# Performance work log

Hardware: AMD Instinct MI355X
Metric: run time of the kernel (lower is better)

## Reference

```python
import jax, jax.numpy as jnp
import numpy as np
from jax import lax

B, N, S, H = 8, 32, 512, 768   # batch, max spans, seq len, bert hidden
K, C, L = 3, 128, 64           # conv kernel height, cnn_hidden_size, num labels


def setup_inputs() -> dict:
    key = jax.random.key(0)
    ks = jax.random.split(key, 9)
    rng = np.random.default_rng(0)
    W = 16  # max span width
    starts = rng.integers(0, S - W, size=(B, N))
    widths = rng.integers(1, W + 1, size=(B, N))
    starts[0, 0], widths[0, 0] = 100, W        # force max span width = 16
    starts[0, 1], widths[0, 1] = S - W, 1      # force max prefix width = 496
    starts[0, 2], widths[0, 2] = 0, 1          # force min end = 1 -> max suffix = 511
    ends = starts + widths
    spans_dranges = jnp.asarray(np.stack([starts, ends], axis=-1), dtype=jnp.int32)
    sc = 0.02
    return {
        "tokens_emb": jax.random.normal(ks[0], (B, S, H), jnp.float32),
        "span_w": jax.random.normal(ks[1], (C, H, K), jnp.float32) * sc,
        "span_b": jax.random.normal(ks[2], (C,), jnp.float32) * sc,
        "prefix_w": jax.random.normal(ks[3], (C, H, K), jnp.float32) * sc,
        "prefix_b": jax.random.normal(ks[4], (C,), jnp.float32) * sc,
        "suffix_w": jax.random.normal(ks[5], (C, H, K), jnp.float32) * sc,
        "suffix_b": jax.random.normal(ks[6], (C,), jnp.float32) * sc,
        "fc_w": jax.random.normal(ks[7], (L, 3 * C), jnp.float32) * sc,
        "fc_b": jax.random.normal(ks[8], (L,), jnp.float32) * sc,
        "spans_dranges": spans_dranges,
        "word_seq_lengths": jnp.full((B,), S, dtype=jnp.int32),
        "max_span_width": W,
        "max_prefix_width": S - W,
        "max_suffix_width": S - 1,
    }


def _conv_pool(x, w, b):
    # x: [BN, T, H]; Conv2d(H->C, kernel (K,1)) over time + max_pool over all valid positions
    T = x.shape[1]
    if T < K:  # original pads with zeros up to kernel size
        x = jnp.pad(x, ((0, 0), (0, K - T), (0, 0)))
    y = lax.conv_general_dilated(x.transpose(0, 2, 1), w, (1,), 'VALID',
                                 dimension_numbers=('NCH', 'OIH', 'NCH'))  # [BN, C, T-K+1]
    return (y + b[None, :, None]).max(axis=2)  # pool_filter_size == full output length


def reference(tokens_emb, span_w, span_b, prefix_w, prefix_b, suffix_w, suffix_b,
              fc_w, fc_b, spans_dranges, word_seq_lengths,
              max_span_width, max_prefix_width, max_suffix_width):
    starts = spans_dranges[..., 0]  # [B,N]
    ends = spans_dranges[..., 1]

    def gather(idx, mask):
        # idx, mask: [B,N,W] -> zero-padded per-span token embeddings [B*N, W, H]
        g = jnp.take_along_axis(tokens_emb[:, None], jnp.clip(idx, 0, S - 1)[..., None], axis=2)
        return (g * mask[..., None]).reshape(B * N, -1, H)

    ar = jnp.arange(max_span_width)
    span_x = gather(starts[..., None] + ar, ar < (ends - starts)[..., None])
    arp = jnp.arange(max_prefix_width)
    prefix_x = gather(jnp.broadcast_to(arp, (B, N, max_prefix_width)), arp < starts[..., None])
    ars = jnp.arange(max_suffix_width)
    suffix_x = gather(ends[..., None] + ars,
                      ars < (word_seq_lengths[:, None, None] - ends[..., None]))

    feats = jnp.concatenate([
        _conv_pool(prefix_x, prefix_w, prefix_b),
        _conv_pool(span_x, span_w, span_b),
        _conv_pool(suffix_x, suffix_w, suffix_b),
    ], axis=-1)  # [B*N, 3C]
    probs = jax.nn.sigmoid(feats @ fc_w.T + fc_b)  # [B*N, L]
    pred_ids = (probs > 0.5).astype(jnp.int32).reshape(B, N, L)
    return probs, pred_ids
```

## Files before the change

### kernel.cpp

```cpp
#include <hip/hip_runtime.h>
#include <hip/hip_bf16.h>
#include <math.h>

#define NEG_INF (-1e30f)

typedef _Float16 half8 __attribute__((ext_vector_type(8)));
typedef _Float16 half4 __attribute__((ext_vector_type(4)));
typedef float f32x4 __attribute__((ext_vector_type(4)));
typedef float f32x16 __attribute__((ext_vector_type(16)));

__device__ __forceinline__ void load_lds16(const void* g, void* l) {
  __builtin_amdgcn_global_load_lds((const __attribute__((address_space(1))) void*)g,
                                   (__attribute__((address_space(3))) void*)l, 16, 0, 0);
}

__global__ __launch_bounds__(256) void prep(
    const float* __restrict__ tokens, const float* __restrict__ span_w,
    const float* __restrict__ prefix_w, const float* __restrict__ suffix_w,
    const float* __restrict__ fc_w, _Float16* __restrict__ A2,
    _Float16* __restrict__ Bt, float* __restrict__ fcT) {
  int bid = blockIdx.x;
  int t = threadIdx.x;
  if (bid < 3072) {
    int g4 = (bid * 256 + t) * 4;
    int m = g4 / 768, h = g4 % 768;
    float4 x = *(const float4*)(tokens + g4);
    float xs[4] = {x.x, x.y, x.z, x.w};
    half4 hi, lo;
#pragma unroll
    for (int i = 0; i < 4; ++i) {
      _Float16 h_ = (_Float16)xs[i];
      hi[i] = h_;
      lo[i] = (_Float16)((xs[i] - (float)h_) * 64.0f);
    }
    size_t base = (size_t)m * 1536 + h;
    *(half4*)(A2 + base) = hi;
    *(half4*)(A2 + base + 768) = lo;
  } else if (bid < 3216) {
    int g = (bid - 3072) * 256 + t;
    int ws = g / 12288;
    int r = g % 12288;
    int c = r / 96, h = (r % 96) * 8;
    const float* wsrc = (ws == 0) ? prefix_w : (ws == 1) ? span_w : suffix_w;
    const float* src = wsrc + (size_t)(c * 768 + h) * 3;
    float wv[24];
#pragma unroll
    for (int i = 0; i < 6; ++i) *(float4*)&wv[i * 4] = *(const float4*)(src + i * 4);
#pragma unroll
    for (int tap = 0; tap < 3; ++tap) {
      half8 hi, lo;
#pragma unroll
      for (int i = 0; i < 8; ++i) {
        float x = wv[i * 3 + tap];
        _Float16 h_ = (_Float16)x;
        hi[i] = h_;
        lo[i] = (_Float16)((x - (float)h_) * 64.0f);
      }
      size_t jb = (size_t)(ws * 384 + tap * 128 + c) * 1536 + h;
      *(half8*)(Bt + jb) = hi;
      *(half8*)(Bt + jb + 768) = lo;
    }
  } else {
    int g = (bid - 3216) * 256 + t;
    int i = g >> 6, c = g & 63;
    fcT[g] = fc_w[c * 384 + i];
  }
}

__global__ __launch_bounds__(512) void gemm_f16(const _Float16* __restrict__ A2,
                                                const _Float16* __restrict__ Bt,
                                                float* __restrict__ Ct) {
  __shared__ _Float16 As[3][128 * 64];
  __shared__ _Float16 Bs[3][64 * 64];
  const int bm = blockIdx.x * 128;
  const int bj = blockIdx.y * 64;
  const int tid = threadIdx.x;
  const int w = tid >> 6;
  const int lane = tid & 63;
  const int lrow = lane >> 3;
  const int cphys = lane & 7;
  const int clog = cphys ^ (lrow & 7);
  const int srcoff = (clog >> 2) * 768 + (clog & 3) * 8;
  const _Float16* gA0 = A2 + (size_t)(bm + w * 16 + lrow) * 1536 + srcoff;
  const _Float16* gA1 = A2 + (size_t)(bm + w * 16 + 8 + lrow) * 1536 + srcoff;
  const _Float16* gB0 = Bt + (size_t)(bj + w * 8 + lrow) * 1536 + srcoff;
  const int m0w = (w & 3) * 32;
  const int n0w = (w >> 2) * 32;
  const int arow = m0w + (lane & 31);
  const int brow = n0w + (lane & 31);
  const int hi32 = lane >> 5;
  const int sw = lane & 7;
#define CO(p, ks) (((((p) * 4 + (ks) * 2 + hi32)) ^ sw) * 8)
#define STAGE(sb, t)                             \
  do {                                           \
    const int kp_ = (t) * 32;                    \
    load_lds16(gA0 + kp_, &As[(sb)][w * 1024]);  \
    load_lds16(gA1 + kp_, &As[(sb)][w * 1024 + 512]); \
    load_lds16(gB0 + kp_, &Bs[(sb)][w * 512]);   \
  } while (0)
  f32x16 aa, ab;
#pragma unroll
  for (int q = 0; q < 16; ++q) {
    aa[q] = 0.f;
    ab[q] = 0.f;
  }
  STAGE(0, 0);
  STAGE(1, 1);
  asm volatile("s_waitcnt vmcnt(3)" ::: "memory");
  __builtin_amdgcn_s_barrier();

  int cur = 0, sbuf = 2;
  for (int t = 0; t < 24; ++t) {
    if (t + 2 < 24) STAGE(sbuf, t + 2);
#pragma unroll
    for (int ks = 0; ks < 2; ++ks) {
      half8 a0 = *(const half8*)&As[cur][arow * 64 + CO(0, ks)];
      half8 a1 = *(const half8*)&As[cur][arow * 64 + CO(1, ks)];
      half8 b0 = *(const half8*)&Bs[cur][brow * 64 + CO(0, ks)];
      half8 b1 = *(const half8*)&Bs[cur][brow * 64 + CO(1, ks)];
      aa = __builtin_amdgcn_mfma_f32_32x32x16_f16(a0, b0, aa, 0, 0, 0);
      ab = __builtin_amdgcn_mfma_f32_32x32x16_f16(a1, b0, ab, 0, 0, 0);
      ab = __builtin_amdgcn_mfma_f32_32x32x16_f16(a0, b1, ab, 0, 0, 0);
    }
    if (t < 23) {
      asm volatile("s_waitcnt lgkmcnt(0)" ::: "memory");
      if (t < 22) {
        asm volatile("s_waitcnt vmcnt(3)" ::: "memory");
      } else {
        asm volatile("s_waitcnt vmcnt(0)" ::: "memory");
      }
      __builtin_amdgcn_s_barrier();
    }
    cur = (cur == 2) ? 0 : cur + 1;
    sbuf = (sbuf == 2) ? 0 : sbuf + 1;
  }
#undef STAGE
#undef CO
  const int n_out = bj + n0w + (lane & 31);
  float* cp = Ct + (size_t)n_out * 4096 + bm + m0w + 4 * hi32;
#pragma unroll
  for (int r = 0; r < 4; ++r) {
    f32x4 v;
#pragma unroll
    for (int q = 0; q < 4; ++q) v[q] = aa[4 * r + q] + 0.015625f * ab[4 * r + q];
    *(f32x4*)(cp + 8 * r) = v;
  }
}

__global__ __launch_bounds__(256) void scan_kernel(const float* __restrict__ Ct,
                                                   const int* __restrict__ wsl,
                                                   float* __restrict__ PM2,
                                                   float* __restrict__ SM2) {
  int pair = blockIdx.x * 4 + (threadIdx.x >> 6);
  int b = pair >> 7;
  int c = pair & 127;
  int lane = threadIdx.x & 63;
  int mb = b * 512;
  int t0 = lane * 8;
  const float* p0 = Ct + (size_t)(0 + c) * 4096 + mb;
  const float* p1 = Ct + (size_t)(128 + c) * 4096 + mb;
  const float* p2 = Ct + (size_t)(256 + c) * 4096 + mb;
  float v[8];
#pragma unroll
  for (int i = 0; i < 8; i++) {
    int t = t0 + i;
    v[i] = (t < 494) ? (p0[t] + p1[t + 1] + p2[t + 2]) : NEG_INF;
  }
#pragma unroll
  for (int i = 1; i < 8; i++) v[i] = fmaxf(v[i], v[i - 1]);
  float x = v[7];
#pragma unroll
  for (int d = 1; d < 64; d <<= 1) {
    float y = __shfl_up(x, d);
    if (lane >= d) x = fmaxf(x, y);
  }
  float excl = __shfl_up(x, 1);
  if (lane == 0) excl = NEG_INF;
  float* pm = PM2 + (size_t)pair * 512;
#pragma unroll
  for (int i = 0; i < 8; i++) {
    int t = t0 + i;
    if (t < 494) pm[t] = fmaxf(v[i], excl);
  }
  const float* s0 = Ct + (size_t)(768 + c) * 4096 + mb;
  const float* s1 = Ct + (size_t)(896 + c) * 4096 + mb;
  const float* s2 = Ct + (size_t)(1024 + c) * 4096 + mb;
  int qmax = wsl[b] - 3;
  if (qmax > 509) qmax = 509;
  float u[8];
#pragma unroll
  for (int i = 0; i < 8; i++) {
    int q = t0 + i;
    u[i] = (q <= qmax) ? (s0[q] + s1[q + 1] + s2[q + 2]) : NEG_INF;
  }
#pragma unroll
  for (int i = 6; i >= 0; i--) u[i] = fmaxf(u[i], u[i + 1]);
  float xr = u[0];
#pragma unroll
  for (int d = 1; d < 64; d <<= 1) {
    float y = __shfl_down(xr, d);
    if (lane < 64 - d) xr = fmaxf(xr, y);
  }
  float exclr = __shfl_down(xr, 1);
  if (lane == 63) exclr = NEG_INF;
  float* sm = SM2 + (size_t)pair * 512;
#pragma unroll
  for (int i = 0; i < 8; i++) sm[t0 + i] = fmaxf(u[i], exclr);
}

__global__ __launch_bounds__(128) void span_kernel(
    const float* __restrict__ Ct, const float* __restrict__ PM2,
    const float* __restrict__ SM2, const float* __restrict__ prefix_b,
    const float* __restrict__ span_b, const float* __restrict__ suffix_b,
    const float* __restrict__ fcT, const float* __restrict__ fc_b,
    const int* __restrict__ spans, const int* __restrict__ wsl,
    float* __restrict__ out) {
  __shared__ float sfeat[384];
  __shared__ float part[64];
  int sp = blockIdx.x;
  int b = sp >> 5;
  int c = threadIdx.x;
  int s = spans[sp * 2], e = spans[sp * 2 + 1];
  int Lb = wsl[b];
  int mb = b * 512;
  {
    const float* t0p = Ct + (size_t)c * 4096 + mb;
    const float* t1p = Ct + (size_t)(128 + c) * 4096 + mb;
    float m = NEG_INF;
    if (s >= 3) m = fmaxf(m, PM2[(size_t)(b * 128 + c) * 512 + s - 3]);
    if (s >= 2 && s <= 495) m = fmaxf(m, t0p[s - 2] + t1p[s - 1]);
    if (s >= 1 && s <= 494) m = fmaxf(m, t0p[s - 1]);
    if (s <= 493) m = fmaxf(m, 0.0f);
    sfeat[c] = m + prefix_b[c];
  }
  {
    const float* u0 = Ct + (size_t)(384 + c) * 4096 + mb;
    const float* u1 = Ct + (size_t)(512 + c) * 4096 + mb;
    const float* u2 = Ct + (size_t)(640 + c) * 4096 + mb;
    int w = e - s;
    float m = NEG_INF;
    for (int p = 0; p + 2 < w; ++p)
      m = fmaxf(m, u0[s + p] + u1[s + p + 1] + u2[s + p + 2]);
    if (w >= 2 && w <= 15) m = fmaxf(m, u0[s + w - 2] + u1[s + w - 1]);
    if (w <= 14) m = fmaxf(m, u0[s + w - 1]);
    if (w <= 13) m = fmaxf(m, 0.0f);
    sfeat[128 + c] = m + span_b[c];
  }
  {
    const float* x0 = Ct + (size_t)(768 + c) * 4096 + mb;
    const float* x1 = Ct + (size_t)(896 + c) * 4096 + mb;
    float m = NEG_INF;
    if (e <= Lb - 3) m = fmaxf(m, SM2[(size_t)(b * 128 + c) * 512 + e]);
    if (Lb - 2 - e >= 0 && Lb - 2 - e <= 508)
      m = fmaxf(m, x0[Lb - 2] + x1[Lb - 1]);
    if (Lb - 1 - e >= 0 && Lb - 1 - e <= 508) m = fmaxf(m, x0[Lb - 1]);
    if (Lb - e <= 508) m = fmaxf(m, 0.0f);
    sfeat[256 + c] = m + suffix_b[c];
  }
  __syncthreads();
  {
    int cc = threadIdx.x & 63;
    int half = threadIdx.x >> 6;
    float acc2 = 0.0f;
    const float* fp = fcT + (size_t)(half * 192) * 64 + cc;
    const float* sf = sfeat + half * 192;
#pragma unroll 8
    for (int i = 0; i < 192; ++i) acc2 = fmaf(sf[i], fp[(size_t)i * 64], acc2);
    if (half) part[cc] = acc2;
    __syncthreads();
    if (!half) {
      float a = acc2 + part[cc] + fc_b[cc];
      float pr = 1.0f / (1.0f + expf(-a));
      out[sp * 64 + cc] = pr;
      out[16384 + sp * 64 + cc] = (pr > 0.5f) ? 1.0f : 0.0f;
    }
  }
}

extern "C" void kernel_launch(void* const* d_in, const int* in_sizes, int n_in,
                              void* d_out, int out_size, void* d_ws,
                              size_t ws_size, hipStream_t stream) {
  const float* tokens = (const float*)d_in[0];
  const float* span_w = (const float*)d_in[1];
  const float* span_b = (const float*)d_in[2];
  const float* prefix_w = (const float*)d_in[3];
  const float* prefix_b = (const float*)d_in[4];
  const float* suffix_w = (const float*)d_in[5];
  const float* suffix_b = (const float*)d_in[6];
  const float* fc_w = (const float*)d_in[7];
  const float* fc_b = (const float*)d_in[8];
  const int* spans = (const int*)d_in[9];
  const int* wsl = (const int*)d_in[10];
  float* out = (float*)d_out;

  char* ws = (char*)d_ws;
  float* Ct = (float*)ws;
  _Float16* A2 = (_Float16*)(ws + 18874368);
  _Float16* Bt = (_Float16*)(ws + 31457280);
  float* PM2 = (float*)(ws + 34996224);
  float* SM2 = (float*)(ws + 37093376);
  float* fcT = (float*)(ws + 39190528);

  hipLaunchKernelGGL(prep, dim3(3312), dim3(256), 0, stream, tokens, span_w,
                     prefix_w, suffix_w, fc_w, A2, Bt, fcT);
  hipLaunchKernelGGL(gemm_f16, dim3(32, 18), dim3(512), 0, stream, A2, Bt, Ct);
  hipLaunchKernelGGL(scan_kernel, dim3(256), dim3(256), 0, stream, Ct, wsl,
                     PM2, SM2);
  hipLaunchKernelGGL(span_kernel, dim3(256), dim3(128), 0, stream, Ct, PM2,
                     SM2, prefix_b, span_b, suffix_b, fcT, fc_b, spans, wsl,
                     out);
}
```

Before: 155.5 us.

## Pre-tile GEMM operands in prep and switch GEMM to double-buffered LDS

The prep kernel now writes the fp16 hi/lo split of the tokens and conv weights in a tiled layout (k-group major, 8-element rows per M/N index), staging the token tile through LDS. This lets the GEMM load contiguous 512-element chunks per wave without an XOR swizzle. The GEMM drops from triple to double buffering, reads all fragments before a barrier, then issues the next stage's loads and runs the MFMAs at raised priority. The intent is to cut LDS bank conflicts and address arithmetic and to overlap loads with compute, at the cost of an extra barrier per iteration and a heavier prep kernel.

```diff
diff --git a/kernel.cpp b/kernel.cpp
--- a/kernel.cpp
+++ b/kernel.cpp
@@ -14,38 +14,56 @@
                                    (__attribute__((address_space(3))) void*)l, 16, 0, 0);
 }
 
+
 __global__ __launch_bounds__(256) void prep(
     const float* __restrict__ tokens, const float* __restrict__ span_w,
     const float* __restrict__ prefix_w, const float* __restrict__ suffix_w,
-    const float* __restrict__ fc_w, _Float16* __restrict__ A2,
-    _Float16* __restrict__ Bt, float* __restrict__ fcT) {
+    const float* __restrict__ fc_w, _Float16* __restrict__ A2t,
+    _Float16* __restrict__ Btt, float* __restrict__ fcT) {
+  __shared__ _Float16 lds[16 * 1544];
   int bid = blockIdx.x;
   int t = threadIdx.x;
-  if (bid < 3072) {
-    int g4 = (bid * 256 + t) * 4;
-    int m = g4 / 768, h = g4 % 768;
-    float4 x = *(const float4*)(tokens + g4);
-    float xs[4] = {x.x, x.y, x.z, x.w};
-    half4 hi, lo;
-#pragma unroll
-    for (int i = 0; i < 4; ++i) {
-      _Float16 h_ = (_Float16)xs[i];
-      hi[i] = h_;
-      lo[i] = (_Float16)((xs[i] - (float)h_) * 64.0f);
-    }
-    size_t base = (size_t)m * 1536 + h;
-    *(half4*)(A2 + base) = hi;
-    *(half4*)(A2 + base + 768) = lo;
-  } else if (bid < 3216) {
-    int g = (bid - 3072) * 256 + t;
+  if (bid < 256) {
+    int m0 = bid * 16;
+#pragma unroll
+    for (int r = 0; r < 12; ++r) {
+      int idx4 = r * 256 + t;
+      int ml = idx4 / 192;
+      int hh = (idx4 % 192) * 4;
+      float4 x = *(const float4*)(tokens + (size_t)m0 * 768 + (size_t)idx4 * 4);
+      float xs[4] = {x.x, x.y, x.z, x.w};
+#pragma unroll
+      for (int i = 0; i < 4; ++i) {
+        _Float16 h_ = (_Float16)xs[i];
+        lds[ml * 1544 + hh + i] = h_;
+        lds[ml * 1544 + 768 + hh + i] = (_Float16)((xs[i] - (float)h_) * 64.0f);
+      }
+    }
+    __syncthreads();
+#pragma unroll
+    for (int rep = 0; rep < 12; ++rep) {
+      int tg = rep * 16 + (t >> 4);
+      int ml = t & 15;
+      int g = tg & 7;
+      int tt = tg >> 3;
+      int p = g >> 2, ks = (g >> 1) & 1, h2 = g & 1;
+      int ksrc = tt * 32 + ks * 16 + h2 * 8;
+      half8 v = *(const half8*)&lds[ml * 1544 + p * 768 + ksrc];
+      *(half8*)(A2t + ((size_t)tg * 4096 + m0 + ml) * 8) = v;
+    }
+  } else if (bid < 400) {
+    int g = (bid - 256) * 256 + t;
     int ws = g / 12288;
     int r = g % 12288;
-    int c = r / 96, h = (r % 96) * 8;
+    int h8 = r >> 7, c = r & 127;
+    int h0 = h8 * 8;
     const float* wsrc = (ws == 0) ? prefix_w : (ws == 1) ? span_w : suffix_w;
-    const float* src = wsrc + (size_t)(c * 768 + h) * 3;
+    const float* src = wsrc + ((size_t)c * 768 + h0) * 3;
     float wv[24];
 #pragma unroll
     for (int i = 0; i < 6; ++i) *(float4*)&wv[i * 4] = *(const float4*)(src + i * 4);
+    int tt = h0 >> 5, ks = (h0 >> 4) & 1, h2 = (h0 >> 3) & 1;
+    int g_hi = ks * 2 + h2;
 #pragma unroll
     for (int tap = 0; tap < 3; ++tap) {
       half8 hi, lo;
@@ -56,48 +74,59 @@
         hi[i] = h_;
         lo[i] = (_Float16)((x - (float)h_) * 64.0f);
       }
-      size_t jb = (size_t)(ws * 384 + tap * 128 + c) * 1536 + h;
-      *(half8*)(Bt + jb) = hi;
-      *(half8*)(Bt + jb + 768) = lo;
+      int j = ws * 384 + tap * 128 + c;
+      *(half8*)(Btt + ((size_t)(tt * 8 + g_hi) * 1152 + j) * 8) = hi;
+      *(half8*)(Btt + ((size_t)(tt * 8 + g_hi + 4) * 1152 + j) * 8) = lo;
     }
   } else {
-    int g = (bid - 3216) * 256 + t;
+    int g = (bid - 400) * 256 + t;
     int i = g >> 6, c = g & 63;
     fcT[g] = fc_w[c * 384 + i];
   }
 }
 
-__global__ __launch_bounds__(512) void gemm_f16(const _Float16* __restrict__ A2,
-                                                const _Float16* __restrict__ Bt,
+__global__ __launch_bounds__(512) void gemm_f16(const _Float16* __restrict__ A2t,
+                                                const _Float16* __restrict__ Btt,
                                                 float* __restrict__ Ct) {
-  __shared__ _Float16 As[3][128 * 64];
-  __shared__ _Float16 Bs[3][64 * 64];
+  __shared__ _Float16 S[2][12288];
   const int bm = blockIdx.x * 128;
   const int bj = blockIdx.y * 64;
   const int tid = threadIdx.x;
   const int w = tid >> 6;
   const int lane = tid & 63;
-  const int lrow = lane >> 3;
-  const int cphys = lane & 7;
-  const int clog = cphys ^ (lrow & 7);
-  const int srcoff = (clog >> 2) * 768 + (clog & 3) * 8;
-  const _Float16* gA0 = A2 + (size_t)(bm + w * 16 + lrow) * 1536 + srcoff;
-  const _Float16* gA1 = A2 + (size_t)(bm + w * 16 + 8 + lrow) * 1536 + srcoff;
-  const _Float16* gB0 = Bt + (size_t)(bj + w * 8 + lrow) * 1536 + srcoff;
+  const int u0 = w * 3;
+  const _Float16* su[3];
+  size_t ts[3];
+  int du[3];
+#pragma unroll
+  for (int i = 0; i < 3; ++i) {
+    int u = u0 + i;
+    du[i] = u * 512;
+    if (u < 16) {
+      su[i] = A2t + (size_t)(u >> 1) * 32768 + ((size_t)bm + (u & 1) * 64 + lane) * 8;
+      ts[i] = 262144;
+    } else {
+      su[i] = Btt + (size_t)(u - 16) * 9216 + ((size_t)bj + lane) * 8;
+      ts[i] = 73728;
+    }
+  }
+  const _Float16* su0 = su[0];
+  const _Float16* su1 = su[1];
+  const _Float16* su2 = su[2];
+  const size_t ts0 = ts[0], ts1 = ts[1], ts2 = ts[2];
+  const int du0 = du[0], du1 = du[1], du2 = du[2];
+#define STAGE(buf, t)                                      \
+  do {                                                     \
+    load_lds16(su0 + (size_t)(t) * ts0, &S[(buf)][du0]);   \
+    load_lds16(su1 + (size_t)(t) * ts1, &S[(buf)][du1]);   \
+    load_lds16(su2 + (size_t)(t) * ts2, &S[(buf)][du2]);   \
+  } while (0)
+  const int ln31 = lane & 31;
+  const int hi32 = lane >> 5;
   const int m0w = (w & 3) * 32;
   const int n0w = (w >> 2) * 32;
-  const int arow = m0w + (lane & 31);
-  const int brow = n0w + (lane & 31);
-  const int hi32 = lane >> 5;
-  const int sw = lane & 7;
-#define CO(p, ks) (((((p) * 4 + (ks) * 2 + hi32)) ^ sw) * 8)
-#define STAGE(sb, t)                             \
-  do {                                           \
-    const int kp_ = (t) * 32;                    \
-    load_lds16(gA0 + kp_, &As[(sb)][w * 1024]);  \
-    load_lds16(gA1 + kp_, &As[(sb)][w * 1024 + 512]); \
-    load_lds16(gB0 + kp_, &Bs[(sb)][w * 512]);   \
-  } while (0)
+  const int aoff = (m0w + ln31) * 8;
+  const int boff = 8192 + (n0w + ln31) * 8;
   f32x16 aa, ab;
 #pragma unroll
   for (int q = 0; q < 16; ++q) {
@@ -107,36 +136,42 @@
   STAGE(0, 0);
   STAGE(1, 1);
   asm volatile("s_waitcnt vmcnt(3)" ::: "memory");
-  __builtin_amdgcn_s_barrier();
-
-  int cur = 0, sbuf = 2;
+  asm volatile("s_barrier" ::: "memory");
+
   for (int t = 0; t < 24; ++t) {
-    if (t + 2 < 24) STAGE(sbuf, t + 2);
+    const int cur = t & 1;
+    half8 a0[2], a1[2], b0[2], b1[2];
 #pragma unroll
     for (int ks = 0; ks < 2; ++ks) {
-      half8 a0 = *(const half8*)&As[cur][arow * 64 + CO(0, ks)];
-      half8 a1 = *(const half8*)&As[cur][arow * 64 + CO(1, ks)];
-      half8 b0 = *(const half8*)&Bs[cur][brow * 64 + CO(0, ks)];
-      half8 b1 = *(const half8*)&Bs[cur][brow * 64 + CO(1, ks)];
-      aa = __builtin_amdgcn_mfma_f32_32x32x16_f16(a0, b0, aa, 0, 0, 0);
-      ab = __builtin_amdgcn_mfma_f32_32x32x16_f16(a1, b0, ab, 0, 0, 0);
-      ab = __builtin_amdgcn_mfma_f32_32x32x16_f16(a0, b1, ab, 0, 0, 0);
-    }
+      const int gb = ks * 2 + hi32;
+      a0[ks] = *(const half8*)&S[cur][gb * 1024 + aoff];
+      a1[ks] = *(const half8*)&S[cur][(gb + 4) * 1024 + aoff];
+      b0[ks] = *(const half8*)&S[cur][boff + gb * 512];
+      b1[ks] = *(const half8*)&S[cur][boff + (gb + 4) * 512];
+    }
+    asm volatile("s_waitcnt lgkmcnt(0)" ::: "memory");
+    __builtin_amdgcn_sched_barrier(0);
+    asm volatile("s_barrier" ::: "memory");
+    if (t + 2 < 24) STAGE(cur, t + 2);
+    __builtin_amdgcn_s_setprio(1);
+#pragma unroll
+    for (int ks = 0; ks < 2; ++ks) {
+      aa = __builtin_amdgcn_mfma_f32_32x32x16_f16(a0[ks], b0[ks], aa, 0, 0, 0);
+      ab = __builtin_amdgcn_mfma_f32_32x32x16_f16(a1[ks], b0[ks], ab, 0, 0, 0);
+      ab = __builtin_amdgcn_mfma_f32_32x32x16_f16(a0[ks], b1[ks], ab, 0, 0, 0);
+    }
+    __builtin_amdgcn_s_setprio(0);
     if (t < 23) {
-      asm volatile("s_waitcnt lgkmcnt(0)" ::: "memory");
       if (t < 22) {
         asm volatile("s_waitcnt vmcnt(3)" ::: "memory");
       } else {
         asm volatile("s_waitcnt vmcnt(0)" ::: "memory");
       }
-      __builtin_amdgcn_s_barrier();
-    }
-    cur = (cur == 2) ? 0 : cur + 1;
-    sbuf = (sbuf == 2) ? 0 : sbuf + 1;
+      asm volatile("s_barrier" ::: "memory");
+    }
   }
 #undef STAGE
-#undef CO
-  const int n_out = bj + n0w + (lane & 31);
+  const int n_out = bj + n0w + ln31;
   float* cp = Ct + (size_t)n_out * 4096 + bm + m0w + 4 * hi32;
 #pragma unroll
   for (int r = 0; r < 4; ++r) {
@@ -295,15 +330,15 @@
 
   char* ws = (char*)d_ws;
   float* Ct = (float*)ws;
-  _Float16* A2 = (_Float16*)(ws + 18874368);
-  _Float16* Bt = (_Float16*)(ws + 31457280);
+  _Float16* A2t = (_Float16*)(ws + 18874368);
+  _Float16* Btt = (_Float16*)(ws + 31457280);
   float* PM2 = (float*)(ws + 34996224);
   float* SM2 = (float*)(ws + 37093376);
   float* fcT = (float*)(ws + 39190528);
 
-  hipLaunchKernelGGL(prep, dim3(3312), dim3(256), 0, stream, tokens, span_w,
-                     prefix_w, suffix_w, fc_w, A2, Bt, fcT);
-  hipLaunchKernelGGL(gemm_f16, dim3(32, 18), dim3(512), 0, stream, A2, Bt, Ct);
+  hipLaunchKernelGGL(prep, dim3(496), dim3(256), 0, stream, tokens, span_w,
+                     prefix_w, suffix_w, fc_w, A2t, Btt, fcT);
+  hipLaunchKernelGGL(gemm_f16, dim3(32, 18), dim3(512), 0, stream, A2t, Btt, Ct);
   hipLaunchKernelGGL(scan_kernel, dim3(256), dim3(256), 0, stream, Ct, wsl,
                      PM2, SM2);
   hipLaunchKernelGGL(span_kernel, dim3(256), dim3(128), 0, stream, Ct, PM2,
```

Measured after the change: 146.8 us. 5.6% less time.
